# Performance work log

Measured on AMD Instinct MI355X. Metric: run time of the kernel, lower is better.

## Reference

```python
import jax, jax.numpy as jnp
import numpy as np

NUM_NODES = 17185
D = 6
FEATS = NUM_NODES * D  # 103110
BATCH = 256
EPS = 1e-5


def setup_inputs() -> dict:
    key = jax.random.key(0)
    ks = jax.random.split(key, 4)
    data = jax.random.normal(ks[0], (BATCH, FEATS), dtype=jnp.float32)
    w_blocks = jax.random.normal(ks[1], (NUM_NODES, D, D), dtype=jnp.float32) * (1.0 / np.sqrt(D))
    b_blocks = jax.random.normal(ks[2], (NUM_NODES, D), dtype=jnp.float32) * 0.1
    fc_w = jax.random.normal(ks[3], (FEATS,), dtype=jnp.float32) * (1.0 / np.sqrt(FEATS))
    return {
        "data": data,
        "w_blocks": w_blocks,
        "b_blocks": b_blocks,
        "bn_gamma": jnp.ones((FEATS,), jnp.float32),
        "bn_beta": jnp.zeros((FEATS,), jnp.float32),
        "bn_mean": jnp.zeros((FEATS,), jnp.float32),
        "bn_var": jnp.ones((FEATS,), jnp.float32),
        "fc_w": fc_w,
        "fc_b": jnp.zeros((1,), jnp.float32),
        "bnf_gamma": jnp.ones((1,), jnp.float32),
        "bnf_beta": jnp.zeros((1,), jnp.float32),
        "bnf_mean": jnp.zeros((1,), jnp.float32),
        "bnf_var": jnp.ones((1,), jnp.float32),
    }


def reference(data, w_blocks, b_blocks, bn_gamma, bn_beta, bn_mean, bn_var,
              fc_w, fc_b, bnf_gamma, bnf_beta, bnf_mean, bnf_var):
    B = data.shape[0]
    # block-diagonal batched matmul replacing 17185 tiny Linear(6,6) calls
    x = data.reshape(B, NUM_NODES, D)                       # [B, N, 6]
    xo = jnp.einsum("bni,noi->bno", x, w_blocks) + b_blocks  # torch Linear: x @ W^T + b
    xo = xo.reshape(B, FEATS)                               # hstack ordering == reshape
    # relu -> BatchNorm1d (eval: running stats) -> dropout (identity in eval)
    h = jnp.maximum(xo, 0.0)
    h = (h - bn_mean) * jax.lax.rsqrt(bn_var + EPS) * bn_gamma + bn_beta
    # final linear [FEATS -> 1], BN(1), sigmoid
    y = h @ fc_w + fc_b                                     # [B]
    y = y[:, None]                                          # [B, 1]
    y = (y - bnf_mean) * jax.lax.rsqrt(bnf_var + EPS) * bnf_gamma + bnf_beta
    return jax.nn.sigmoid(y)
```

## Files before the change

### kernel.cpp

```cpp
#include <hip/hip_runtime.h>
#include <stdint.h>

#define NUM_NODES 17185
#define DD 6
#define FEATS (NUM_NODES * DD)
#define BATCH 256
#define EPS 1e-5f

#define NC 256
#define BC 8
#define NCHUNK ((NUM_NODES + NC - 1) / NC)

__device__ float g_pm[NCHUNK * 256];
__device__ float g_pc[NCHUNK];

__global__ __launch_bounds__(NC) void main_kernel(
    const float* __restrict__ data, const float* __restrict__ wb, const float* __restrict__ bb,
    const float* __restrict__ gamma, const float* __restrict__ var, const float* __restrict__ fcw,
    const float* __restrict__ beta, const float* __restrict__ mean) {

    const int tid = threadIdx.x;
    const int n = blockIdx.x * NC + tid;
    const bool valid = (n < NUM_NODES);

    float wreg[36], bias[6], a[6];
    #pragma unroll
    for (int k = 0; k < 36; k++) wreg[k] = 0.f;
    #pragma unroll
    for (int k = 0; k < 6; k++) { bias[k] = 0.f; a[k] = 0.f; }

    float cnode = 0.f;

    if (valid) {
        const float4* wp = (const float4*)(wb + (size_t)n * 36);
        #pragma unroll
        for (int k = 0; k < 9; k++) {
            float4 v = wp[k];
            wreg[4*k] = v.x; wreg[4*k+1] = v.y; wreg[4*k+2] = v.z; wreg[4*k+3] = v.w;
        }
        const float2* bp = (const float2*)(bb + (size_t)n * 6);
        #pragma unroll
        for (int k = 0; k < 3; k++) { float2 v = bp[k]; bias[2*k] = v.x; bias[2*k+1] = v.y; }
        const int f0 = n * 6;
        const float2* gp = (const float2*)(gamma + f0);
        const float2* vp = (const float2*)(var + f0);
        const float2* fp = (const float2*)(fcw + f0);
        float fw[6];
        #pragma unroll
        for (int k = 0; k < 3; k++) {
            float2 g = gp[k], v = vp[k], f = fp[k];
            fw[2*k] = f.x; fw[2*k+1] = f.y;
            a[2*k]   = g.x * rsqrtf(v.x + EPS) * f.x;
            a[2*k+1] = g.y * rsqrtf(v.y + EPS) * f.y;
        }
        if (blockIdx.y == 0) {
            const float2* bep = (const float2*)(beta + f0);
            const float2* mp  = (const float2*)(mean + f0);
            #pragma unroll
            for (int k = 0; k < 3; k++) {
                float2 be = bep[k], m = mp[k];
                cnode += be.x * fw[2*k]   - m.x * a[2*k];
                cnode += be.y * fw[2*k+1] - m.y * a[2*k+1];
            }
        }
    }

    const int b0 = blockIdx.y * BC;
    float acc[BC];
    #pragma unroll
    for (int r = 0; r < BC; r++) acc[r] = 0.f;

    if (valid) {
        const float2* xbase = (const float2*)(data + (size_t)b0 * FEATS + (size_t)n * 6);
        #pragma unroll
        for (int r = 0; r < BC; r++) {
            const float2* xp = xbase + (size_t)r * (FEATS / 2);
            float2 u0 = xp[0], u1 = xp[1], u2 = xp[2];
            float x0 = u0.x, x1 = u0.y, x2 = u1.x, x3 = u1.y, x4 = u2.x, x5 = u2.y;
            #pragma unroll
            for (int o = 0; o < 6; o++) {
                float s = bias[o];
                s = fmaf(x0, wreg[o*6+0], s);
                s = fmaf(x1, wreg[o*6+1], s);
                s = fmaf(x2, wreg[o*6+2], s);
                s = fmaf(x3, wreg[o*6+3], s);
                s = fmaf(x4, wreg[o*6+4], s);
                s = fmaf(x5, wreg[o*6+5], s);
                acc[r] = fmaf(fmaxf(s, 0.f), a[o], acc[r]);
            }
        }
    }

    __shared__ float red[4][BC];
    #pragma unroll
    for (int r = 0; r < BC; r++) {
        float v = acc[r];
        #pragma unroll
        for (int off = 32; off; off >>= 1) v += __shfl_down(v, off);
        if ((tid & 63) == 0) red[tid >> 6][r] = v;
    }

    if (blockIdx.y == 0) {
        float v = cnode;
        #pragma unroll
        for (int off = 32; off; off >>= 1) v += __shfl_down(v, off);
        __shared__ float credd[4];
        if ((tid & 63) == 0) credd[tid >> 6] = v;
        __syncthreads();
        if (tid == 0) g_pc[blockIdx.x] = credd[0] + credd[1] + credd[2] + credd[3];
    } else {
        __syncthreads();
    }

    if (tid < BC) {
        float s = red[0][tid] + red[1][tid] + red[2][tid] + red[3][tid];
        g_pm[blockIdx.x * 256 + b0 + tid] = s;
    }
}

__global__ __launch_bounds__(256) void final_kernel(
    const float* __restrict__ fcb, const float* __restrict__ bnfg,
    const float* __restrict__ bnfb, const float* __restrict__ bnfm,
    const float* __restrict__ bnfv, float* __restrict__ out) {
    const int b = threadIdx.x;

    float c = (b < NCHUNK) ? g_pc[b] : 0.f;
    #pragma unroll
    for (int off = 32; off; off >>= 1) c += __shfl_down(c, off);
    __shared__ float red[4];
    if ((b & 63) == 0) red[b >> 6] = c;
    __syncthreads();
    const float c_sum = red[0] + red[1] + red[2] + red[3];

    float y = 0.f;
    #pragma unroll 4
    for (int ch = 0; ch < NCHUNK; ch++) y += g_pm[ch * 256 + b];

    y += c_sum + fcb[0];
    float sc = bnfg[0] * rsqrtf(bnfv[0] + EPS);
    float z = (y - bnfm[0]) * sc + bnfb[0];
    out[b] = 1.f / (1.f + expf(-z));
}

extern "C" void kernel_launch(void* const* d_in, const int* in_sizes, int n_in,
                              void* d_out, int out_size, void* d_ws, size_t ws_size,
                              hipStream_t stream) {
    const float* data  = (const float*)d_in[0];
    const float* wb    = (const float*)d_in[1];
    const float* bb    = (const float*)d_in[2];
    const float* gamma = (const float*)d_in[3];
    const float* beta  = (const float*)d_in[4];
    const float* mean  = (const float*)d_in[5];
    const float* var   = (const float*)d_in[6];
    const float* fcw   = (const float*)d_in[7];
    const float* fcb   = (const float*)d_in[8];
    const float* bnfg  = (const float*)d_in[9];
    const float* bnfb  = (const float*)d_in[10];
    const float* bnfm  = (const float*)d_in[11];
    const float* bnfv  = (const float*)d_in[12];
    (void)d_ws; (void)ws_size;

    dim3 grid(NCHUNK, BATCH / BC);
    main_kernel<<<grid, NC, 0, stream>>>(data, wb, bb, gamma, var, fcw, beta, mean);

    final_kernel<<<1, 256, 0, stream>>>(fcb, bnfg, bnfb, bnfm, bnfv, (float*)d_out);
}
```

Baseline: 190.2 us.

## Split each node's six outputs across two threads per node

Each block now runs 512 threads, and two threads share one node. Each thread computes three of the six outputs, so it holds half the weight rows and half the per-feature scale terms. The goal is more parallelism and fewer registers per thread to raise occupancy. The cost is that both threads load the same 6 input values per batch row, duplicating reads (probably served from cache), and the reductions now span 8 waves instead of 4.

```diff
diff --git a/kernel.cpp b/kernel.cpp
--- a/kernel.cpp
+++ b/kernel.cpp
@@ -8,60 +8,48 @@
 #define EPS 1e-5f
 
 #define NC 256
+#define NT 512
 #define BC 8
 #define NCHUNK ((NUM_NODES + NC - 1) / NC)
 
 __device__ float g_pm[NCHUNK * 256];
 __device__ float g_pc[NCHUNK];
 
-__global__ __launch_bounds__(NC) void main_kernel(
+__global__ __launch_bounds__(NT) void main_kernel(
     const float* __restrict__ data, const float* __restrict__ wb, const float* __restrict__ bb,
     const float* __restrict__ gamma, const float* __restrict__ var, const float* __restrict__ fcw,
     const float* __restrict__ beta, const float* __restrict__ mean) {
 
     const int tid = threadIdx.x;
-    const int n = blockIdx.x * NC + tid;
+    const int nl  = tid & 255;
+    const int h   = tid >> 8;
+    const int n   = blockIdx.x * NC + nl;
     const bool valid = (n < NUM_NODES);
 
-    float wreg[36], bias[6], a[6];
+    float wreg[18], bias[3], a3[3];
     #pragma unroll
-    for (int k = 0; k < 36; k++) wreg[k] = 0.f;
+    for (int k = 0; k < 18; k++) wreg[k] = 0.f;
     #pragma unroll
-    for (int k = 0; k < 6; k++) { bias[k] = 0.f; a[k] = 0.f; }
+    for (int k = 0; k < 3; k++) { bias[k] = 0.f; a3[k] = 0.f; }
 
     float cnode = 0.f;
 
     if (valid) {
-        const float4* wp = (const float4*)(wb + (size_t)n * 36);
+        const float2* wp = (const float2*)(wb + (size_t)n * 36 + h * 18);
         #pragma unroll
         for (int k = 0; k < 9; k++) {
-            float4 v = wp[k];
-            wreg[4*k] = v.x; wreg[4*k+1] = v.y; wreg[4*k+2] = v.z; wreg[4*k+3] = v.w;
+            float2 v = wp[k];
+            wreg[2*k] = v.x; wreg[2*k+1] = v.y;
         }
-        const float2* bp = (const float2*)(bb + (size_t)n * 6);
+        const int f0 = n * 6 + h * 3;
         #pragma unroll
-        for (int k = 0; k < 3; k++) { float2 v = bp[k]; bias[2*k] = v.x; bias[2*k+1] = v.y; }
-        const int f0 = n * 6;
-        const float2* gp = (const float2*)(gamma + f0);
-        const float2* vp = (const float2*)(var + f0);
-        const float2* fp = (const float2*)(fcw + f0);
-        float fw[6];
-        #pragma unroll
-        for (int k = 0; k < 3; k++) {
-            float2 g = gp[k], v = vp[k], f = fp[k];
-            fw[2*k] = f.x; fw[2*k+1] = f.y;
-            a[2*k]   = g.x * rsqrtf(v.x + EPS) * f.x;
-            a[2*k+1] = g.y * rsqrtf(v.y + EPS) * f.y;
-        }
-        if (blockIdx.y == 0) {
-            const float2* bep = (const float2*)(beta + f0);
-            const float2* mp  = (const float2*)(mean + f0);
-            #pragma unroll
-            for (int k = 0; k < 3; k++) {
-                float2 be = bep[k], m = mp[k];
-                cnode += be.x * fw[2*k]   - m.x * a[2*k];
-                cnode += be.y * fw[2*k+1] - m.y * a[2*k+1];
-            }
+        for (int j = 0; j < 3; j++) {
+            bias[j] = bb[f0 + j];
+            float fw = fcw[f0 + j];
+            float aj = gamma[f0 + j] * rsqrtf(var[f0 + j] + EPS) * fw;
+            a3[j] = aj;
+            if (blockIdx.y == 0)
+                cnode += beta[f0 + j] * fw - mean[f0 + j] * aj;
         }
     }
 
@@ -78,42 +66,50 @@
             float2 u0 = xp[0], u1 = xp[1], u2 = xp[2];
             float x0 = u0.x, x1 = u0.y, x2 = u1.x, x3 = u1.y, x4 = u2.x, x5 = u2.y;
             #pragma unroll
-            for (int o = 0; o < 6; o++) {
-                float s = bias[o];
-                s = fmaf(x0, wreg[o*6+0], s);
-                s = fmaf(x1, wreg[o*6+1], s);
-                s = fmaf(x2, wreg[o*6+2], s);
-                s = fmaf(x3, wreg[o*6+3], s);
-                s = fmaf(x4, wreg[o*6+4], s);
-                s = fmaf(x5, wreg[o*6+5], s);
-                acc[r] = fmaf(fmaxf(s, 0.f), a[o], acc[r]);
+            for (int j = 0; j < 3; j++) {
+                float s = bias[j];
+                s = fmaf(x0, wreg[j*6+0], s);
+                s = fmaf(x1, wreg[j*6+1], s);
+                s = fmaf(x2, wreg[j*6+2], s);
+                s = fmaf(x3, wreg[j*6+3], s);
+                s = fmaf(x4, wreg[j*6+4], s);
+                s = fmaf(x5, wreg[j*6+5], s);
+                acc[r] = fmaf(fmaxf(s, 0.f), a3[j], acc[r]);
             }
         }
     }
 
-    __shared__ float red[4][BC];
+    __shared__ float red[8][BC];
+    const int w = tid >> 6;
     #pragma unroll
     for (int r = 0; r < BC; r++) {
         float v = acc[r];
         #pragma unroll
         for (int off = 32; off; off >>= 1) v += __shfl_down(v, off);
-        if ((tid & 63) == 0) red[tid >> 6][r] = v;
+        if ((tid & 63) == 0) red[w][r] = v;
     }
 
     if (blockIdx.y == 0) {
         float v = cnode;
         #pragma unroll
         for (int off = 32; off; off >>= 1) v += __shfl_down(v, off);
-        __shared__ float credd[4];
-        if ((tid & 63) == 0) credd[tid >> 6] = v;
+        __shared__ float credd[8];
+        if ((tid & 63) == 0) credd[w] = v;
         __syncthreads();
-        if (tid == 0) g_pc[blockIdx.x] = credd[0] + credd[1] + credd[2] + credd[3];
+        if (tid == 0) {
+            float s = 0.f;
+            #pragma unroll
+            for (int k = 0; k < 8; k++) s += credd[k];
+            g_pc[blockIdx.x] = s;
+        }
     } else {
         __syncthreads();
     }
 
     if (tid < BC) {
-        float s = red[0][tid] + red[1][tid] + red[2][tid] + red[3][tid];
+        float s = 0.f;
+        #pragma unroll
+        for (int k = 0; k < 8; k++) s += red[k][tid];
         g_pm[blockIdx.x * 256 + b0 + tid] = s;
     }
 }
@@ -161,7 +157,7 @@
     (void)d_ws; (void)ws_size;
 
     dim3 grid(NCHUNK, BATCH / BC);
-    main_kernel<<<grid, NC, 0, stream>>>(data, wb, bb, gamma, var, fcw, beta, mean);
+    main_kernel<<<grid, NT, 0, stream>>>(data, wb, bb, gamma, var, fcw, beta, mean);
 
     final_kernel<<<1, 256, 0, stream>>>(fcb, bnfg, bnfb, bnfm, bnfv, (float*)d_out);
 }
```

Result: slower. 209.0 us (+9.9%).
